# Performance work log

Measured on AMD Instinct MI355X. Metric: run time of the kernel, lower is better.

## Reference

```python
import jax, jax.numpy as jnp
import numpy as np
from functools import partial

STRIDES = (8, 16, 32, 64)
SCORE_T = 0.25
NMS_T = 0.45
MAX_DET = 300
PRE_NMS_K = 512  # fixed candidate budget replacing data-dependent torch.where


def _decode_level(cls, reg, kpt, stride):
    # cls: (C,H,W), reg: (4,H,W), kpt: (10,H,W) for one image, one level
    score = jax.nn.sigmoid(cls).max(axis=0)               # (H,W) max over classes
    H, W = score.shape
    ys, xs = jnp.meshgrid(jnp.arange(H, dtype=cls.dtype),
                          jnp.arange(W, dtype=cls.dtype), indexing='ij')
    cx = (xs + 0.5) * stride
    cy = (ys + 0.5) * stride
    cxd = cx + reg[0] * stride
    cyd = cy + reg[1] * stride
    w = jnp.exp(reg[2]) * stride
    h = jnp.exp(reg[3]) * stride
    boxes = jnp.stack([cxd - w / 2, cyd - h / 2, cxd + w / 2, cyd + h / 2], axis=-1)
    boxes = boxes.reshape(-1, 4)                           # (HW,4) xyxy
    kx = cx[None] + kpt[0::2] * stride                     # (5,H,W)
    ky = cy[None] + kpt[1::2] * stride                     # (5,H,W)
    kpts = jnp.stack([kx, ky], axis=-1)                    # (5,H,W,2)
    kpts = kpts.transpose(1, 2, 0, 3).reshape(-1, 5, 2)    # (HW,5,2)
    return boxes, score.reshape(-1), kpts


def _pairwise_iou(b):
    # b: (K,4) xyxy -> (K,K) IoU, same convention as torchvision.ops.nms
    x1 = jnp.maximum(b[:, None, 0], b[None, :, 0])
    y1 = jnp.maximum(b[:, None, 1], b[None, :, 1])
    x2 = jnp.minimum(b[:, None, 2], b[None, :, 2])
    y2 = jnp.minimum(b[:, None, 3], b[None, :, 3])
    inter = jnp.clip(x2 - x1, 0) * jnp.clip(y2 - y1, 0)
    area = (b[:, 2] - b[:, 0]) * (b[:, 3] - b[:, 1])
    union = area[:, None] + area[None, :] - inter
    return inter / jnp.maximum(union, 1e-9)


def _nms_keep(boxes, valid):
    # boxes sorted by descending score; greedy NMS via suppression sweep
    K = boxes.shape[0]
    ious = _pairwise_iou(boxes)
    idx = jnp.arange(K)

    def body(i, keep):
        sup = keep[i] & (ious[i] > NMS_T) & (idx > i)
        return keep & ~sup

    return jax.lax.fori_loop(0, K, body, valid)


def _per_image(boxes, scores, kpts):
    # boxes (N,4), scores (N,), kpts (N,5,2) concatenated over all levels
    masked = jnp.where(scores > SCORE_T, scores, 0.0)      # score-threshold mask
    top_s, top_i = jax.lax.top_k(masked, PRE_NMS_K)        # sorted descending
    b = boxes[top_i]                                       # (K,4)
    k = kpts[top_i]                                        # (K,5,2)
    valid = top_s > SCORE_T
    keep = _nms_keep(b, valid)
    # compact kept detections (in score order) into first MAX_DET slots
    rank = jnp.cumsum(keep) - 1
    slot = jnp.where(keep & (rank < MAX_DET), rank, MAX_DET)
    feat = jnp.concatenate([b, top_s[:, None], k.reshape(PRE_NMS_K, 10)], axis=1)  # (K,15)
    buf = jnp.zeros((MAX_DET + 1, 15), feat.dtype).at[slot].set(feat)
    return buf[:MAX_DET]                                   # (MAX_DET, 15): [x1,y1,x2,y2,score,kpts*10]


def setup_inputs() -> dict:
    key = jax.random.key(0)
    B = 16
    sizes = (256, 128, 64, 32)
    keys = jax.random.split(key, 12)
    inp = {}
    for li, s in enumerate(sizes):
        inp[f'cls{li}'] = jax.random.normal(keys[li], (B, 1, s, s), jnp.float32)
        inp[f'reg{li}'] = jax.random.normal(keys[4 + li], (B, 4, s, s), jnp.float32)
        inp[f'kpt{li}'] = jax.random.normal(keys[8 + li], (B, 10, s, s), jnp.float32)
    return inp


def reference(cls0, cls1, cls2, cls3, reg0, reg1, reg2, reg3, kpt0, kpt1, kpt2, kpt3):
    clss = (cls0, cls1, cls2, cls3)
    regs = (reg0, reg1, reg2, reg3)
    kpts = (kpt0, kpt1, kpt2, kpt3)
    bs, ss, ks = [], [], []
    for c, r, k, stride in zip(clss, regs, kpts, STRIDES):
        dec = jax.vmap(partial(_decode_level, stride=stride))
        b, s, kp = dec(c, r, k)
        bs.append(b); ss.append(s); ks.append(kp)
    boxes = jnp.concatenate(bs, axis=1)    # (B, N, 4)
    scores = jnp.concatenate(ss, axis=1)   # (B, N)
    keypts = jnp.concatenate(ks, axis=1)   # (B, N, 5, 2)
    return jax.vmap(_per_image)(boxes, scores, keypts)  # (B, MAX_DET, 15)
```

## Files before the change

### kernel.cpp

```cpp
#include <hip/hip_runtime.h>
#include <stdint.h>

#define CAP_   2048
#define KSEL   512
#define MAXDET 300
#define NIMG   16
#define SCORE_T 0.25f
#define NMS_T   0.45f
#define HBINS  72
#define SLICES 8
#define PERSLICE 2720
#define RCH    64


__device__ __forceinline__ float sigmoidf_(float x) {
  return 1.0f / (1.0f + expf(-x));
}

__device__ __forceinline__ float4 load_cls4_(const float* c0, const float* c1,
                                             const float* c2, const float* c3,
                                             int b, int g) {
  if (g < 16384) return ((const float4*)(c0 + (size_t)b * 65536))[g];
  if (g < 20480) return ((const float4*)(c1 + (size_t)b * 16384))[g - 16384];
  if (g < 21504) return ((const float4*)(c2 + (size_t)b * 4096))[g - 20480];
  return ((const float4*)(c3 + (size_t)b * 1024))[g - 21504];
}

__global__ __launch_bounds__(1024)
void k_scan(const float* __restrict__ c0, const float* __restrict__ c1,
            const float* __restrict__ c2, const float* __restrict__ c3,
            uint32_t* __restrict__ histS, uint32_t* __restrict__ cnt) {
  const int b = blockIdx.x >> 3;
  const int slice = blockIdx.x & 7;
  const int tid = threadIdx.x;
  const int wave = tid >> 6;

  __shared__ uint32_t lh[16][HBINS];
  for (int i = tid; i < 16 * HBINS; i += 1024) ((uint32_t*)lh)[i] = 0;
  __syncthreads();

  for (int it = 0; it < 3; ++it) {
    int lg = it * 1024 + tid;
    if (lg < PERSLICE) {
      int g = slice * PERSLICE + lg;
      float4 v = load_cls4_(c0, c1, c2, c3, b, g);
      float sv[4] = {v.x, v.y, v.z, v.w};
#pragma unroll
      for (int e = 0; e < 4; ++e) {
        float s = sigmoidf_(sv[e]);
        if (s > SCORE_T) {
          uint32_t bin = (__float_as_uint(s) >> 18) - 4000u;
          if (bin > 64u) bin = 64u;
          atomicAdd(&lh[wave][bin], 1u);
        }
      }
    }
  }
  __syncthreads();

  if (tid < HBINS) {
    uint32_t s = 0;
#pragma unroll
    for (int w = 0; w < 16; ++w) s += lh[w][tid];
    histS[blockIdx.x * HBINS + tid] = s;
  }
  if (blockIdx.x == 0 && tid < NIMG) cnt[tid] = 0;
}

__global__ __launch_bounds__(1024)
void k_compact(const float* __restrict__ c0, const float* __restrict__ c1,
               const float* __restrict__ c2, const float* __restrict__ c3,
               const uint32_t* __restrict__ histS,
               uint32_t* __restrict__ cnt, uint64_t* __restrict__ keys) {
  const int b = blockIdx.x >> 3;
  const int slice = blockIdx.x & 7;
  const int tid = threadIdx.x;

  __shared__ uint64_t lk[CAP_];
  __shared__ uint32_t lcnt;
  __shared__ uint32_t gbase;
  __shared__ uint32_t s_tot[HBINS];
  __shared__ uint32_t s_thrv;

  if (tid == 0) lcnt = 0;
  if (tid < HBINS) {
    uint32_t s = 0;
#pragma unroll
    for (int sl = 0; sl < SLICES; ++sl)
      s += histS[(b * SLICES + sl) * HBINS + tid];
    s_tot[tid] = s;
  }
  __syncthreads();

  if (tid < 64) {
    uint32_t x = s_tot[tid];
    if (tid == 63) x += s_tot[64];
    for (int off = 1; off < 64; off <<= 1) {
      uint32_t v = __shfl_down(x, off);
      if (tid + off < 64) x += v;
    }
    uint32_t nxt = __shfl_down(x, 1);
    if (tid == 63) nxt = 0;
    bool cross = (x >= KSEL) && (nxt < KSEL);
    unsigned long long m = __ballot(cross);
    if (tid == 0) {
      int bucket = m ? (__ffsll(m) - 1) : 0;
      s_thrv = ((uint32_t)(4000 + bucket)) << 18;
    }
  }
  __syncthreads();

  const uint32_t tb = s_thrv;

  for (int it = 0; it < 3; ++it) {
    int lg = it * 1024 + tid;
    if (lg < PERSLICE) {
      int g = slice * PERSLICE + lg;
      float4 v = load_cls4_(c0, c1, c2, c3, b, g);
      float sv[4] = {v.x, v.y, v.z, v.w};
#pragma unroll
      for (int e = 0; e < 4; ++e) {
        float s = sigmoidf_(sv[e]);
        if (s > SCORE_T) {
          uint32_t bits = __float_as_uint(s);
          if (bits >= tb) {
            uint32_t n = (uint32_t)(4 * g + e);
            uint32_t p = atomicAdd(&lcnt, 1u);
            if (p < CAP_)
              lk[p] = ((uint64_t)bits << 32) | (0xFFFFFFFFu - n);
          }
        }
      }
    }
  }
  __syncthreads();

  if (tid == 0) {
    uint32_t c = lcnt > CAP_ ? CAP_ : lcnt;
    gbase = atomicAdd(&cnt[b], c);
  }
  __syncthreads();

  uint32_t c = lcnt > CAP_ ? CAP_ : lcnt;
  for (uint32_t i = tid; i < c; i += 1024) {
    uint32_t pos = gbase + i;
    if (pos < CAP_) keys[(size_t)b * CAP_ + pos] = lk[i];
  }
}

__global__ __launch_bounds__(1024)
void k_rank(const uint64_t* __restrict__ keys, const uint32_t* __restrict__ cnt,
            const float* __restrict__ r0p, const float* __restrict__ r1p,
            const float* __restrict__ r2p, const float* __restrict__ r3p,
            uint64_t* __restrict__ skeys, float* __restrict__ bxs) {
  const int b = blockIdx.x >> 5;
  const int chunk = blockIdx.x & 31;
  const int t = threadIdx.x;

  __shared__ __align__(16) uint64_t lkey[CAP_];
  __shared__ uint32_t part[RCH][17];

  int c = (int)cnt[b];
  if (c > CAP_) c = CAP_;
  if (chunk != 0 && chunk * RCH >= c) return;

  for (int i = t; i < CAP_; i += 1024)
    lkey[i] = (i < c) ? keys[(size_t)b * CAP_ + i] : 0ull;
  __syncthreads();

  const int ci   = t & (RCH - 1);
  const int seg  = t >> 6;
  const int cand = chunk * RCH + ci;
  const uint64_t mykey = lkey[cand];
  const int hi2 = (c + 1) >> 1;
  int j2beg = seg * 64;
  int j2end = j2beg + 64; if (j2end > hi2) j2end = hi2;
  uint32_t pc = 0;
  const ulonglong2* lk2 = (const ulonglong2*)lkey;
#pragma unroll 4
  for (int j2 = j2beg; j2 < j2end; ++j2) {
    ulonglong2 kk = lk2[j2];
    pc += (kk.x > mykey) ? 1u : 0u;
    pc += (kk.y > mykey) ? 1u : 0u;
  }
  part[ci][seg] = pc;
  __syncthreads();

  if (t < RCH) {
    int rank = 0;
#pragma unroll
    for (int s = 0; s < 16; ++s) rank += part[t][s];
    int cand0 = chunk * RCH + t;
    if (cand0 < c && rank < KSEL) {
      uint64_t key = lkey[cand0];
      float sc = __uint_as_float((uint32_t)(key >> 32));
      float x1 = 0.f, y1 = 0.f, x2 = 0.f, y2 = 0.f;
      if (sc > SCORE_T) {
        int n = (int)(0xFFFFFFFFu - (uint32_t)key);
        const float* rp; int local, Nl, logW; float st;
        if (n < 65536)      { rp = r0p + (size_t)b * 4 * 65536; local = n;          Nl = 65536; logW = 8; st = 8.f;  }
        else if (n < 81920) { rp = r1p + (size_t)b * 4 * 16384; local = n - 65536;  Nl = 16384; logW = 7; st = 16.f; }
        else if (n < 86016) { rp = r2p + (size_t)b * 4 * 4096;  local = n - 81920;  Nl = 4096;  logW = 6; st = 32.f; }
        else                { rp = r3p + (size_t)b * 4 * 1024;  local = n - 86016;  Nl = 1024;  logW = 5; st = 64.f; }
        int y = local >> logW, x = local & ((1 << logW) - 1);
        float cx = ((float)x + 0.5f) * st;
        float cy = ((float)y + 0.5f) * st;
        float rv0 = rp[local];
        float rv1 = rp[Nl + local];
        float rv2 = rp[2 * Nl + local];
        float rv3 = rp[3 * Nl + local];
        float cxd = cx + rv0 * st;
        float cyd = cy + rv1 * st;
        float w = expf(rv2) * st;
        float h = expf(rv3) * st;
        x1 = cxd - w * 0.5f; y1 = cyd - h * 0.5f;
        x2 = cxd + w * 0.5f; y2 = cyd + h * 0.5f;
      }
      skeys[(size_t)b * KSEL + rank] = key;
      float* base = bxs + (size_t)b * 5 * KSEL;
      base[rank]            = x1;
      base[KSEL + rank]     = y1;
      base[2 * KSEL + rank] = x2;
      base[3 * KSEL + rank] = y2;
      base[4 * KSEL + rank] = (x2 - x1) * (y2 - y1);
    }
  }

  if (chunk == 0) {
    int slot = t - 512;
    if (slot >= 0 && slot < KSEL && slot >= c) {
      skeys[(size_t)b * KSEL + slot] = 0ull;
      float* base = bxs + (size_t)b * 5 * KSEL;
      base[slot]            = 0.f;
      base[KSEL + slot]     = 0.f;
      base[2 * KSEL + slot] = 0.f;
      base[3 * KSEL + slot] = 0.f;
      base[4 * KSEL + slot] = 0.f;
    }
  }
}

__global__ __launch_bounds__(512)
void k_sup(const float* __restrict__ bxs, uint64_t* __restrict__ supT) {
  const int b = blockIdx.x >> 3, chunk = blockIdx.x & 7;
  const int tid = threadIdx.x, wave = tid >> 6, lane = tid & 63;

  __shared__ float sx1[KSEL], sy1[KSEL], sx2[KSEL], sy2[KSEL], sar[KSEL];
  const float* base = bxs + (size_t)b * 5 * KSEL;
  sx1[tid] = base[tid];
  sy1[tid] = base[KSEL + tid];
  sx2[tid] = base[2 * KSEL + tid];
  sy2[tid] = base[3 * KSEL + tid];
  sar[tid] = base[4 * KSEL + tid];
  __syncthreads();

  for (int task = wave; task < 512; task += 8) {
    int i = (chunk << 6) + (task >> 3);
    int w = task & 7;
    int jj = (w << 6) | lane;
    float xx1 = fmaxf(sx1[i], sx1[jj]);
    float yy1 = fmaxf(sy1[i], sy1[jj]);
    float xx2 = fminf(sx2[i], sx2[jj]);
    float yy2 = fminf(sy2[i], sy2[jj]);
    float inter = fmaxf(xx2 - xx1, 0.f) * fmaxf(yy2 - yy1, 0.f);
    float uni = sar[i] + sar[jj] - inter;
    float iou = inter / fmaxf(uni, 1e-9f);
    bool pred = (jj < i) && (iou > NMS_T);
    unsigned long long word = __ballot(pred);
    if (lane == 0) supT[((size_t)b * KSEL + i) * 8 + w] = word;
  }
}

__global__ __launch_bounds__(512)
void k_sweep(const uint64_t* __restrict__ skeys, const float* __restrict__ bxs,
             const uint64_t* __restrict__ supT,
             const float* __restrict__ p0, const float* __restrict__ p1,
             const float* __restrict__ p2, const float* __restrict__ p3,
             float* __restrict__ out) {
  const int b = blockIdx.x;
  const int t = threadIdx.x;
  const int wave = t >> 6, lane = t & 63;

  __shared__ uint64_t keepS[8];

  const uint64_t* rp_ = supT + ((size_t)b * KSEL + t) * 8;
  uint64_t row0 = rp_[0], row1 = rp_[1], row2 = rp_[2], row3 = rp_[3],
           row4 = rp_[4], row5 = rp_[5], row6 = rp_[6], row7 = rp_[7];

  uint64_t key = skeys[(size_t)b * KSEL + t];
  float sc = __uint_as_float((uint32_t)(key >> 32));
  bool valid = sc > SCORE_T;

  uint64_t myintra;
  switch (wave) {
    case 0: myintra = row0; break; case 1: myintra = row1; break;
    case 2: myintra = row2; break; case 3: myintra = row3; break;
    case 4: myintra = row4; break; case 5: myintra = row5; break;
    case 6: myintra = row6; break; default: myintra = row7; break;
  }

  bool extsup = false;

#define STAGE(CH, ROWCH)                                                   \
  {                                                                        \
    if (wave == CH) {                                                      \
      uint64_t a = __ballot(valid && !extsup);                             \
      while (true) {                                                       \
        bool nk = valid && !extsup && ((myintra & a) == 0ull);             \
        uint64_t a2 = __ballot(nk);                                        \
        if (a2 == a) break;                                                \
        a = a2;                                                            \
      }                                                                    \
      if (lane == 0) keepS[CH] = a;                                        \
    }                                                                      \
    __syncthreads();                                                       \
    { uint64_t kch = keepS[CH];                                            \
      extsup = extsup || ((ROWCH & kch) != 0ull); }                        \
  }

  STAGE(0, row0)
  STAGE(1, row1)
  STAGE(2, row2)
  STAGE(3, row3)
  STAGE(4, row4)
  STAGE(5, row5)
  STAGE(6, row6)
  STAGE(7, row7)
#undef STAGE

  uint64_t f0 = keepS[0], f1 = keepS[1], f2 = keepS[2], f3 = keepS[3],
           f4 = keepS[4], f5 = keepS[5], f6 = keepS[6], f7 = keepS[7];
  int ntot = __popcll(f0) + __popcll(f1) + __popcll(f2) + __popcll(f3) +
             __popcll(f4) + __popcll(f5) + __popcll(f6) + __popcll(f7);
  int nwrite = ntot > MAXDET ? MAXDET : ntot;

  {
    int w = wave, bit = lane;
    uint64_t myw;
    switch (w) {
      case 0: myw = f0; break; case 1: myw = f1; break;
      case 2: myw = f2; break; case 3: myw = f3; break;
      case 4: myw = f4; break; case 5: myw = f5; break;
      case 6: myw = f6; break; default: myw = f7; break;
    }
    bool kept = (myw >> bit) & 1ull;
    if (kept) {
      uint64_t pref[8] = {f0, f1, f2, f3, f4, f5, f6, f7};
      int r = 0;
#pragma unroll
      for (int u = 0; u < 8; ++u) {
        if (u < w) r += __popcll(pref[u]);
        else if (u == w) r += __popcll(pref[u] & ((bit == 0) ? 0ull : ((1ull << bit) - 1ull)));
      }
      if (r < MAXDET) {
        int n = (int)(0xFFFFFFFFu - (uint32_t)key);
        const float* kp; int local, Nl, logW; float st;
        if (n < 65536)      { kp = p0 + (size_t)b * 10 * 65536; local = n;          Nl = 65536; logW = 8; st = 8.f;  }
        else if (n < 81920) { kp = p1 + (size_t)b * 10 * 16384; local = n - 65536;  Nl = 16384; logW = 7; st = 16.f; }
        else if (n < 86016) { kp = p2 + (size_t)b * 10 * 4096;  local = n - 81920;  Nl = 4096;  logW = 6; st = 32.f; }
        else                { kp = p3 + (size_t)b * 10 * 1024;  local = n - 86016;  Nl = 1024;  logW = 5; st = 64.f; }
        int y = local >> logW, x = local & ((1 << logW) - 1);
        float cx = ((float)x + 0.5f) * st;
        float cy = ((float)y + 0.5f) * st;
        const float* bb = bxs + (size_t)b * 5 * KSEL;
        float* o = out + ((size_t)b * MAXDET + r) * 15;
        o[0] = bb[t];
        o[1] = bb[KSEL + t];
        o[2] = bb[2 * KSEL + t];
        o[3] = bb[3 * KSEL + t];
        o[4] = sc;
#pragma unroll
        for (int q = 0; q < 5; ++q) {
          float kx = cx + kp[(2 * q) * Nl + local] * st;
          float ky = cy + kp[(2 * q + 1) * Nl + local] * st;
          o[5 + 2 * q] = kx;
          o[6 + 2 * q] = ky;
        }
      }
    }
  }

  if (t < MAXDET && t >= nwrite) {
    float* o = out + ((size_t)b * MAXDET + t) * 15;
#pragma unroll
    for (int e = 0; e < 15; ++e) o[e] = 0.f;
  }
}

extern "C" void kernel_launch(void* const* d_in, const int* in_sizes, int n_in,
                              void* d_out, int out_size, void* d_ws, size_t ws_size,
                              hipStream_t stream) {
  const float* cls0 = (const float*)d_in[0];
  const float* reg0 = (const float*)d_in[1];
  const float* kpt0 = (const float*)d_in[2];
  const float* cls1 = (const float*)d_in[3];
  const float* reg1 = (const float*)d_in[4];
  const float* kpt1 = (const float*)d_in[5];
  const float* cls2 = (const float*)d_in[6];
  const float* reg2 = (const float*)d_in[7];
  const float* kpt2 = (const float*)d_in[8];
  const float* cls3 = (const float*)d_in[9];
  const float* reg3 = (const float*)d_in[10];
  const float* kpt3 = (const float*)d_in[11];
  float* out = (float*)d_out;

  uint8_t* ws = (uint8_t*)d_ws;
  uint32_t* histS = (uint32_t*)ws;
  float*    bxs   = (float*)   ws;
  uint32_t* cnt   = (uint32_t*)(ws + 163840);
  uint64_t* skeys = (uint64_t*)(ws + 163904);
  uint64_t* keys  = (uint64_t*)(ws + 229440);
  uint64_t* supT  = (uint64_t*)(ws + 229440);

  k_scan<<<NIMG * SLICES, 1024, 0, stream>>>(cls0, cls1, cls2, cls3, histS, cnt);
  k_compact<<<NIMG * SLICES, 1024, 0, stream>>>(cls0, cls1, cls2, cls3, histS, cnt, keys);
  k_rank<<<NIMG * 32, 1024, 0, stream>>>(keys, cnt, reg0, reg1, reg2, reg3, skeys, bxs);
  k_sup<<<NIMG * 8, 512, 0, stream>>>(bxs, supT);
  k_sweep<<<NIMG, 512, 0, stream>>>(skeys, bxs, supT,
                                    kpt0, kpt1, kpt2, kpt3, out);
}
```

Baseline: 42.13 us.

## Fuse suppression-matrix and NMS sweep kernels into one per-image block

Merges the IoU suppression-bitmask kernel and the greedy sweep kernel into a single 1024-thread block per image, keeping the bitmask and boxes in shared memory. This removes one kernel launch and the global-memory write and read of the suppression matrix. In exchange, the IoU matrix is computed by only 16 blocks instead of 128, so that phase has less parallelism across compute units.

Result: slower. 91.52 us (+117.2%).

```diff
diff --git a/kernel.cpp b/kernel.cpp
--- a/kernel.cpp
+++ b/kernel.cpp
@@ -240,23 +240,33 @@
   }
 }
 
-__global__ __launch_bounds__(512)
-void k_sup(const float* __restrict__ bxs, uint64_t* __restrict__ supT) {
-  const int b = blockIdx.x >> 3, chunk = blockIdx.x & 7;
-  const int tid = threadIdx.x, wave = tid >> 6, lane = tid & 63;
+__global__ __launch_bounds__(1024)
+void k_supsweep(const uint64_t* __restrict__ skeys, const float* __restrict__ bxs,
+                const float* __restrict__ p0, const float* __restrict__ p1,
+                const float* __restrict__ p2, const float* __restrict__ p3,
+                float* __restrict__ out) {
+  const int b = blockIdx.x;
+  const int t = threadIdx.x;
+  const int wave = t >> 6, lane = t & 63;
 
   __shared__ float sx1[KSEL], sy1[KSEL], sx2[KSEL], sy2[KSEL], sar[KSEL];
-  const float* base = bxs + (size_t)b * 5 * KSEL;
-  sx1[tid] = base[tid];
-  sy1[tid] = base[KSEL + tid];
-  sx2[tid] = base[2 * KSEL + tid];
-  sy2[tid] = base[3 * KSEL + tid];
-  sar[tid] = base[4 * KSEL + tid];
-  __syncthreads();
-
-  for (int task = wave; task < 512; task += 8) {
-    int i = (chunk << 6) + (task >> 3);
-    int w = task & 7;
+  __shared__ uint64_t skey[KSEL];
+  __shared__ uint64_t ssup[KSEL][9];
+  __shared__ uint64_t keepS[8];
+
+  if (t < KSEL) {
+    const float* base = bxs + (size_t)b * 5 * KSEL;
+    sx1[t] = base[t];
+    sy1[t] = base[KSEL + t];
+    sx2[t] = base[2 * KSEL + t];
+    sy2[t] = base[3 * KSEL + t];
+    sar[t] = base[4 * KSEL + t];
+    skey[t] = skeys[(size_t)b * KSEL + t];
+  }
+  __syncthreads();
+
+  for (int task = wave; task < KSEL * 8; task += 16) {
+    int i = task >> 3, w = task & 7;
     int jj = (w << 6) | lane;
     float xx1 = fmaxf(sx1[i], sx1[jj]);
     float yy1 = fmaxf(sy1[i], sy1[jj]);
@@ -267,38 +277,27 @@
     float iou = inter / fmaxf(uni, 1e-9f);
     bool pred = (jj < i) && (iou > NMS_T);
     unsigned long long word = __ballot(pred);
-    if (lane == 0) supT[((size_t)b * KSEL + i) * 8 + w] = word;
-  }
-}
-
-__global__ __launch_bounds__(512)
-void k_sweep(const uint64_t* __restrict__ skeys, const float* __restrict__ bxs,
-             const uint64_t* __restrict__ supT,
-             const float* __restrict__ p0, const float* __restrict__ p1,
-             const float* __restrict__ p2, const float* __restrict__ p3,
-             float* __restrict__ out) {
-  const int b = blockIdx.x;
-  const int t = threadIdx.x;
-  const int wave = t >> 6, lane = t & 63;
-
-  __shared__ uint64_t keepS[8];
-
-  const uint64_t* rp_ = supT + ((size_t)b * KSEL + t) * 8;
-  uint64_t row0 = rp_[0], row1 = rp_[1], row2 = rp_[2], row3 = rp_[3],
-           row4 = rp_[4], row5 = rp_[5], row6 = rp_[6], row7 = rp_[7];
-
-  uint64_t key = skeys[(size_t)b * KSEL + t];
-  float sc = __uint_as_float((uint32_t)(key >> 32));
-  bool valid = sc > SCORE_T;
-
-  uint64_t myintra;
-  switch (wave) {
-    case 0: myintra = row0; break; case 1: myintra = row1; break;
-    case 2: myintra = row2; break; case 3: myintra = row3; break;
-    case 4: myintra = row4; break; case 5: myintra = row5; break;
-    case 6: myintra = row6; break; default: myintra = row7; break;
-  }
-
+    if (lane == 0) ssup[i][w] = word;
+  }
+  __syncthreads();
+
+  uint64_t row0 = 0, row1 = 0, row2 = 0, row3 = 0,
+           row4 = 0, row5 = 0, row6 = 0, row7 = 0;
+  uint64_t key = 0; float sc = 0.f; bool valid = false;
+  uint64_t myintra = 0;
+  if (t < KSEL) {
+    row0 = ssup[t][0]; row1 = ssup[t][1]; row2 = ssup[t][2]; row3 = ssup[t][3];
+    row4 = ssup[t][4]; row5 = ssup[t][5]; row6 = ssup[t][6]; row7 = ssup[t][7];
+    key = skey[t];
+    sc = __uint_as_float((uint32_t)(key >> 32));
+    valid = sc > SCORE_T;
+    switch (wave) {
+      case 0: myintra = row0; break; case 1: myintra = row1; break;
+      case 2: myintra = row2; break; case 3: myintra = row3; break;
+      case 4: myintra = row4; break; case 5: myintra = row5; break;
+      case 6: myintra = row6; break; default: myintra = row7; break;
+    }
+  }
   bool extsup = false;
 
 #define STAGE(CH, ROWCH)                                                   \
@@ -334,7 +333,7 @@
              __popcll(f4) + __popcll(f5) + __popcll(f6) + __popcll(f7);
   int nwrite = ntot > MAXDET ? MAXDET : ntot;
 
-  {
+  if (t < KSEL) {
     int w = wave, bit = lane;
     uint64_t myw;
     switch (w) {
@@ -362,12 +361,8 @@
         int y = local >> logW, x = local & ((1 << logW) - 1);
         float cx = ((float)x + 0.5f) * st;
         float cy = ((float)y + 0.5f) * st;
-        const float* bb = bxs + (size_t)b * 5 * KSEL;
         float* o = out + ((size_t)b * MAXDET + r) * 15;
-        o[0] = bb[t];
-        o[1] = bb[KSEL + t];
-        o[2] = bb[2 * KSEL + t];
-        o[3] = bb[3 * KSEL + t];
+        o[0] = sx1[t]; o[1] = sy1[t]; o[2] = sx2[t]; o[3] = sy2[t];
         o[4] = sc;
 #pragma unroll
         for (int q = 0; q < 5; ++q) {
@@ -410,12 +405,10 @@
   uint32_t* cnt   = (uint32_t*)(ws + 163840);
   uint64_t* skeys = (uint64_t*)(ws + 163904);
   uint64_t* keys  = (uint64_t*)(ws + 229440);
-  uint64_t* supT  = (uint64_t*)(ws + 229440);
 
   k_scan<<<NIMG * SLICES, 1024, 0, stream>>>(cls0, cls1, cls2, cls3, histS, cnt);
   k_compact<<<NIMG * SLICES, 1024, 0, stream>>>(cls0, cls1, cls2, cls3, histS, cnt, keys);
   k_rank<<<NIMG * 32, 1024, 0, stream>>>(keys, cnt, reg0, reg1, reg2, reg3, skeys, bxs);
-  k_sup<<<NIMG * 8, 512, 0, stream>>>(bxs, supT);
-  k_sweep<<<NIMG, 512, 0, stream>>>(skeys, bxs, supT,
-                                    kpt0, kpt1, kpt2, kpt3, out);
-}
+  k_supsweep<<<NIMG, 1024, 0, stream>>>(skeys, bxs,
+                                        kpt0, kpt1, kpt2, kpt3, out);
+}
```
